# Kernel tuning notes

Measured on AMD Instinct MI355X. Metric: run time of the kernel, lower is better.

Reference implementation:

```python
import jax, jax.numpy as jnp
import numpy as np

NEG_INF = -1e9

def setup_inputs() -> dict:
    key = jax.random.key(0)
    k1, k2, k3, k4, k5 = jax.random.split(key, 5)
    B, Lq, Lk, D = 8, 2048, 2048, 256
    query = jax.random.normal(k1, (B, Lq, D), dtype=jnp.float32)
    key_t = jax.random.normal(k2, (B, Lk, D), dtype=jnp.float32)
    value = jax.random.normal(k3, (B, Lk, D), dtype=jnp.float32)
    mask = jax.random.randint(k4, (B, Lq, Lk), 0, 2, dtype=jnp.int32)
    # nn.Linear(d_k, 1, bias=False) weight, flattened to [d_k]
    w_align = jax.random.normal(k5, (D,), dtype=jnp.float32) / jnp.sqrt(jnp.float32(D))
    return {"query": query, "key": key_t, "value": value, "mask": mask, "w_align": w_align}

def reference(query, key, value, mask, w_align):
    # Bahdanau additive scores: w . (q_i + k_j). Since the alignment layer is
    # linear, distribute it: score[b,i,j] = (q[b,i] . w) + (k[b,j] . w),
    # avoiding the [B,Lq,Lk,D] broadcast intermediate (same math exactly).
    sq = jnp.einsum('bqd,d->bq', query, w_align)   # [B,Lq]
    sk = jnp.einsum('bkd,d->bk', key, w_align)     # [B,Lk]
    scores = sq[:, :, None] + sk[:, None, :]       # [B,Lq,Lk]
    scores = jnp.where(mask == 0, NEG_INF, scores)
    p_attn = jax.nn.softmax(scores, axis=-1)
    return jnp.matmul(p_attn, value)               # [B,Lq,Dv]
```

## Files before the change

### kernel.cpp

```cpp
#include <hip/hip_runtime.h>
#include <hip/hip_bf16.h>


#define NB 8
#define LQ 2048
#define LK 2048
#define DD 256

typedef __attribute__((ext_vector_type(8))) short short8v;
typedef __attribute__((ext_vector_type(8))) unsigned short ushort8v;
typedef __attribute__((ext_vector_type(4))) float f32x4;

__device__ inline unsigned short f2bf(float x) {
  union { __hip_bfloat16 h; unsigned short u; } cv;
  cv.h = __float2bfloat16(x);
  return cv.u;
}

__device__ inline uint4 pack_mask8(const int4 a, const int4 b) {
  uint4 p;
  p.x = (a.x ? 0x3F80u : 0u) | (a.y ? 0x3F800000u : 0u);
  p.y = (a.z ? 0x3F80u : 0u) | (a.w ? 0x3F800000u : 0u);
  p.z = (b.x ? 0x3F80u : 0u) | (b.y ? 0x3F800000u : 0u);
  p.w = (b.z ? 0x3F80u : 0u) | (b.w ? 0x3F800000u : 0u);
  return p;
}

__global__ __launch_bounds__(256) void bah_precompute(
    const float* __restrict__ key, const float* __restrict__ value,
    const float* __restrict__ w, unsigned short* __restrict__ evB,
    unsigned short* __restrict__ eb)
{
  __shared__ float e_s[32];
  __shared__ unsigned short t_s[32][260];

  const int t = threadIdx.x;
  const int lane = t & 63;
  const int wid = t >> 6;
  const int blk = blockIdx.x;
  const int b = blk & 7;
  const int ks = blk >> 3;
  const int j0 = ks * 32;

  const float4 wv4 = reinterpret_cast<const float4*>(w)[lane];

#pragma unroll
  for (int r8 = 0; r8 < 8; ++r8) {
    const int r = wid * 8 + r8;
    const size_t row = (size_t)b * LK + j0 + r;
    const float4 kv = reinterpret_cast<const float4*>(key + row * DD)[lane];
    float s = kv.x * wv4.x + kv.y * wv4.y + kv.z * wv4.z + kv.w * wv4.w;
#pragma unroll
    for (int off = 32; off; off >>= 1) s += __shfl_xor(s, off);
    const float e = __expf(s);
    if (lane == 0) { e_s[r] = e; eb[row] = f2bf(e); }
  }
  __syncthreads();

#pragma unroll
  for (int g = 0; g < 8; ++g) {
    const int jr = g * 4 + wid;
    const int d0 = lane * 4;
    const size_t row = (size_t)b * LK + j0 + jr;
    const float4 vv = reinterpret_cast<const float4*>(value + row * DD)[lane];
    const float e = e_s[jr];
    ushort4 u;
    u.x = f2bf(e * vv.x);
    u.y = f2bf(e * vv.y);
    u.z = f2bf(e * vv.z);
    u.w = f2bf(e * vv.w);
    *reinterpret_cast<ushort4*>(&t_s[jr][d0]) = u;
  }
  __syncthreads();

  const int lr = lane & 15;
  const int lj = lane >> 4;
#pragma unroll
  for (int n4 = 0; n4 < 4; ++n4) {
    const int n = wid * 4 + n4;
    ushort8v va;
#pragma unroll
    for (int i = 0; i < 8; ++i) va[i] = t_s[lj * 8 + i][n * 16 + lr];
    *reinterpret_cast<ushort8v*>(
        evB + ((size_t)((b * 64 + ks) * 16 + n) * 64 + lane) * 8) = va;
  }
}

__global__ __launch_bounds__(256, 2) void bah_gemm(
    const int* __restrict__ mask, const unsigned short* __restrict__ evB,
    const unsigned short* __restrict__ eb, float* __restrict__ out)
{
  __shared__ unsigned short A_s[4][32 * 64];
  __shared__ float denom_s[32];

  const int t = threadIdx.x;
  const int lane = t & 63;
  const int wq = t >> 6;
  const int lr = lane & 15;
  const int lj = lane >> 4;

  const int blk = blockIdx.x;
  const int b = blk & 7;
  const int i0 = (blk >> 3) * 32;

  const int rw = wq * 8 + (lane & 7);
  const int cw = lane >> 3;
  const int* amask = mask + ((size_t)b * LQ + i0 + rw) * LK + cw * 8;
  const int awr = rw * 64 + ((cw ^ (rw & 7)) * 8);

  const unsigned short* bB[4];
#pragma unroll
  for (int n = 0; n < 4; ++n)
    bB[n] = evB + ((size_t)(b * 1024 + (4 * wq + n)) * 64 + lane) * 8;
  const unsigned short* ebb = eb + b * 2048 + lj * 8;

  const int af00 = lr * 64 + (((0 + lj) ^ (lr & 7)) * 8);
  const int af01 = lr * 64 + (((4 + lj) ^ (lr & 7)) * 8);
  const int af10 = (16 + lr) * 64 + (((0 + lj) ^ ((16 + lr) & 7)) * 8);
  const int af11 = (16 + lr) * 64 + (((4 + lj) ^ ((16 + lr) & 7)) * 8);

  f32x4 acc[2][4] = {};
  f32x4 accd0 = {}, accd1 = {};
  const short8v z8 = {};

  {
    const int4 p0 = *reinterpret_cast<const int4*>(amask + 0);
    const int4 p1 = *reinterpret_cast<const int4*>(amask + 4);
    *reinterpret_cast<uint4*>(&A_s[0][awr]) = pack_mask8(p0, p1);
  }
  int4 aC0 = *reinterpret_cast<const int4*>(amask + 64);
  int4 aC1 = *reinterpret_cast<const int4*>(amask + 68);
  __syncthreads();

#pragma unroll 4
  for (int tt = 0; tt < 32; ++tt) {
    const int bufC = tt & 3;
    const int bufW = (tt + 1) & 3;

    short8v bf0[4], bf1[4];
#pragma unroll
    for (int n = 0; n < 4; ++n) {
      bf0[n] = *reinterpret_cast<const short8v*>(bB[n] + (size_t)(2 * tt + 0) * 8192);
      bf1[n] = *reinterpret_cast<const short8v*>(bB[n] + (size_t)(2 * tt + 1) * 8192);
    }
    short8v ef0 = z8, ef1 = z8;
    if (wq == 0) {
      const short8v e0 = *reinterpret_cast<const short8v*>(ebb + (2 * tt + 0) * 32);
      const short8v e1 = *reinterpret_cast<const short8v*>(ebb + (2 * tt + 1) * 32);
      ef0 = (lr == 0) ? e0 : z8;
      ef1 = (lr == 0) ? e1 : z8;
    }
    const int k2 = ((tt + 2) & 31) * 64;
    const int4 aN0 = *reinterpret_cast<const int4*>(amask + k2);
    const int4 aN1 = *reinterpret_cast<const int4*>(amask + k2 + 4);
    __builtin_amdgcn_sched_barrier(0);

    *reinterpret_cast<uint4*>(&A_s[bufW][awr]) = pack_mask8(aC0, aC1);
    asm volatile("s_waitcnt lgkmcnt(0)" ::: "memory");
    __builtin_amdgcn_sched_barrier(0);
    __builtin_amdgcn_s_barrier();
    __builtin_amdgcn_sched_barrier(0);

#pragma unroll
    for (int h = 0; h < 2; ++h) {
      const short8v a0 = *reinterpret_cast<const short8v*>(&A_s[bufC][h ? af01 : af00]);
      const short8v a1 = *reinterpret_cast<const short8v*>(&A_s[bufC][h ? af11 : af10]);
      if (wq == 0) {
        const short8v efh = h ? ef1 : ef0;
        accd0 = __builtin_amdgcn_mfma_f32_16x16x32_bf16(a0, efh, accd0, 0, 0, 0);
        accd1 = __builtin_amdgcn_mfma_f32_16x16x32_bf16(a1, efh, accd1, 0, 0, 0);
      }
#pragma unroll
      for (int n = 0; n < 4; ++n) {
        const short8v bv = h ? bf1[n] : bf0[n];
        acc[0][n] = __builtin_amdgcn_mfma_f32_16x16x32_bf16(a0, bv, acc[0][n], 0, 0, 0);
        acc[1][n] = __builtin_amdgcn_mfma_f32_16x16x32_bf16(a1, bv, acc[1][n], 0, 0, 0);
      }
    }
    aC0 = aN0; aC1 = aN1;
  }

  if (wq == 0 && lr == 0) {
#pragma unroll
    for (int r = 0; r < 4; ++r) {
      denom_s[lj * 4 + r] = accd0[r];
      denom_s[16 + lj * 4 + r] = accd1[r];
    }
  }
  __syncthreads();

#pragma unroll
  for (int m = 0; m < 2; ++m) {
    const int row0 = m * 16 + lj * 4;
    float inv[4];
#pragma unroll
    for (int r = 0; r < 4; ++r) {
      const float dn = denom_s[row0 + r];
      inv[r] = (dn != 0.f) ? 1.f / dn : 0.f;
    }
#pragma unroll
    for (int n = 0; n < 4; ++n) {
      const int col = wq * 64 + n * 16 + lr;
#pragma unroll
      for (int r = 0; r < 4; ++r)
        out[((size_t)b * LQ + (i0 + row0 + r)) * DD + col] = acc[m][n][r] * inv[r];
    }
  }
}

extern "C" void kernel_launch(void* const* d_in, const int* in_sizes, int n_in,
                              void* d_out, int out_size, void* d_ws, size_t ws_size,
                              hipStream_t stream) {
  const float* key   = (const float*)d_in[1];
  const float* value = (const float*)d_in[2];
  const int*   mask  = (const int*)d_in[3];
  const float* w     = (const float*)d_in[4];
  float* out = (float*)d_out;

  unsigned short* evB = (unsigned short*)d_ws;
  unsigned short* eb  = (unsigned short*)((char*)d_ws + (size_t)NB * DD * LK * 2);

  bah_precompute<<<NB * (LK / 32), 256, 0, stream>>>(key, value, w, evB, eb);
  bah_gemm<<<NB * (LQ / 32), 256, 0, stream>>>(mask, evB, eb, out);
}
```

Measured before the change: 55.07 us.

## Split GEMM over key dimension with atomic accumulation and separate normalization pass

The GEMM now uses 64-row tiles with 8 waves (2x4 wave grid) per block and splits the 2048-long key reduction into two halves handled by separate blocks. Partial numerators and denominators are combined with float atomicAdd into the zeroed output and a workspace denominator buffer. A new divide kernel then normalizes each row. This gives more B-operand reuse per block, at the cost of two memsets, atomic traffic on the full output, an extra read-write pass, and non-deterministic summation order.

```diff
diff --git a/kernel.cpp b/kernel.cpp
--- a/kernel.cpp
+++ b/kernel.cpp
@@ -86,57 +86,69 @@
   }
 }
 
-__global__ __launch_bounds__(256, 2) void bah_gemm(
+__global__ __launch_bounds__(512, 4) void bah_gemm(
     const int* __restrict__ mask, const unsigned short* __restrict__ evB,
-    const unsigned short* __restrict__ eb, float* __restrict__ out)
+    const unsigned short* __restrict__ eb, float* __restrict__ out,
+    float* __restrict__ denom)
 {
-  __shared__ unsigned short A_s[4][32 * 64];
-  __shared__ float denom_s[32];
+  __shared__ unsigned short A_s[3][64 * 64];
 
   const int t = threadIdx.x;
   const int lane = t & 63;
-  const int wq = t >> 6;
+  const int wid = t >> 6;
+  const int wm = wid >> 2;
+  const int wn = wid & 3;
   const int lr = lane & 15;
   const int lj = lane >> 4;
 
   const int blk = blockIdx.x;
   const int b = blk & 7;
-  const int i0 = (blk >> 3) * 32;
-
-  const int rw = wq * 8 + (lane & 7);
-  const int cw = lane >> 3;
-  const int* amask = mask + ((size_t)b * LQ + i0 + rw) * LK + cw * 8;
-  const int awr = rw * 64 + ((cw ^ (rw & 7)) * 8);
+  const int r = blk >> 3;
+  const int i0 = (r & 31) * 64;
+  const int s = r >> 5;
+  const int kb = s * 1024;
+
+  const int sr = t >> 3;
+  const int c8 = t & 7;
+  const int* aptr = mask + ((size_t)b * LQ + i0 + sr) * LK + kb + c8 * 8;
+  const int awr = sr * 64 + ((c8 ^ (sr & 7)) * 8);
 
   const unsigned short* bB[4];
 #pragma unroll
   for (int n = 0; n < 4; ++n)
-    bB[n] = evB + ((size_t)(b * 1024 + (4 * wq + n)) * 64 + lane) * 8;
-  const unsigned short* ebb = eb + b * 2048 + lj * 8;
-
-  const int af00 = lr * 64 + (((0 + lj) ^ (lr & 7)) * 8);
-  const int af01 = lr * 64 + (((4 + lj) ^ (lr & 7)) * 8);
-  const int af10 = (16 + lr) * 64 + (((0 + lj) ^ ((16 + lr) & 7)) * 8);
-  const int af11 = (16 + lr) * 64 + (((4 + lj) ^ ((16 + lr) & 7)) * 8);
+    bB[n] = evB + ((size_t)(b * 64 + kb / 32) * 16 + wn * 4 + n) * 512 + lane * 8;
+  const unsigned short* ebb = eb + b * LK + kb + lj * 8;
+
+  int afo[2][2];
+#pragma unroll
+  for (int m = 0; m < 2; ++m) {
+    const int row = wm * 32 + m * 16 + lr;
+#pragma unroll
+    for (int h = 0; h < 2; ++h)
+      afo[m][h] = row * 64 + (((4 * h + lj) ^ (row & 7)) * 8);
+  }
 
   f32x4 acc[2][4] = {};
-  f32x4 accd0 = {}, accd1 = {};
+  f32x4 accd[2] = {};
   const short8v z8 = {};
 
   {
-    const int4 p0 = *reinterpret_cast<const int4*>(amask + 0);
-    const int4 p1 = *reinterpret_cast<const int4*>(amask + 4);
+    const int4 p0 = *reinterpret_cast<const int4*>(aptr);
+    const int4 p1 = *reinterpret_cast<const int4*>(aptr + 4);
     *reinterpret_cast<uint4*>(&A_s[0][awr]) = pack_mask8(p0, p1);
   }
-  int4 aC0 = *reinterpret_cast<const int4*>(amask + 64);
-  int4 aC1 = *reinterpret_cast<const int4*>(amask + 68);
+  int4 aC0 = *reinterpret_cast<const int4*>(aptr + 64);
+  int4 aC1 = *reinterpret_cast<const int4*>(aptr + 68);
   __syncthreads();
 
-#pragma unroll 4
-  for (int tt = 0; tt < 32; ++tt) {
-    const int bufC = tt & 3;
-    const int bufW = (tt + 1) & 3;
-
+#pragma unroll 3
+  for (int tt = 0; tt < 16; ++tt) {
+    const int bufC = tt % 3;
+    const int bufW = (tt + 1) % 3;
+
+    const int k2 = ((tt + 2) & 15) * 64;
+    const int4 aN0 = *reinterpret_cast<const int4*>(aptr + k2);
+    const int4 aN1 = *reinterpret_cast<const int4*>(aptr + k2 + 4);
     short8v bf0[4], bf1[4];
 #pragma unroll
     for (int n = 0; n < 4; ++n) {
@@ -144,15 +156,10 @@
       bf1[n] = *reinterpret_cast<const short8v*>(bB[n] + (size_t)(2 * tt + 1) * 8192);
     }
     short8v ef0 = z8, ef1 = z8;
-    if (wq == 0) {
-      const short8v e0 = *reinterpret_cast<const short8v*>(ebb + (2 * tt + 0) * 32);
-      const short8v e1 = *reinterpret_cast<const short8v*>(ebb + (2 * tt + 1) * 32);
-      ef0 = (lr == 0) ? e0 : z8;
-      ef1 = (lr == 0) ? e1 : z8;
-    }
-    const int k2 = ((tt + 2) & 31) * 64;
-    const int4 aN0 = *reinterpret_cast<const int4*>(amask + k2);
-    const int4 aN1 = *reinterpret_cast<const int4*>(amask + k2 + 4);
+    if (wn == 0 && lr == 0) {
+      ef0 = *reinterpret_cast<const short8v*>(ebb + tt * 64);
+      ef1 = *reinterpret_cast<const short8v*>(ebb + tt * 64 + 32);
+    }
     __builtin_amdgcn_sched_barrier(0);
 
     *reinterpret_cast<uint4*>(&A_s[bufW][awr]) = pack_mask8(aC0, aC1);
@@ -163,12 +170,12 @@
 
 #pragma unroll
     for (int h = 0; h < 2; ++h) {
-      const short8v a0 = *reinterpret_cast<const short8v*>(&A_s[bufC][h ? af01 : af00]);
-      const short8v a1 = *reinterpret_cast<const short8v*>(&A_s[bufC][h ? af11 : af10]);
-      if (wq == 0) {
+      const short8v a0 = *reinterpret_cast<const short8v*>(&A_s[bufC][afo[0][h]]);
+      const short8v a1 = *reinterpret_cast<const short8v*>(&A_s[bufC][afo[1][h]]);
+      if (wn == 0) {
         const short8v efh = h ? ef1 : ef0;
-        accd0 = __builtin_amdgcn_mfma_f32_16x16x32_bf16(a0, efh, accd0, 0, 0, 0);
-        accd1 = __builtin_amdgcn_mfma_f32_16x16x32_bf16(a1, efh, accd1, 0, 0, 0);
+        accd[0] = __builtin_amdgcn_mfma_f32_16x16x32_bf16(a0, efh, accd[0], 0, 0, 0);
+        accd[1] = __builtin_amdgcn_mfma_f32_16x16x32_bf16(a1, efh, accd[1], 0, 0, 0);
       }
 #pragma unroll
       for (int n = 0; n < 4; ++n) {
@@ -180,32 +187,40 @@
     aC0 = aN0; aC1 = aN1;
   }
 
-  if (wq == 0 && lr == 0) {
-#pragma unroll
-    for (int r = 0; r < 4; ++r) {
-      denom_s[lj * 4 + r] = accd0[r];
-      denom_s[16 + lj * 4 + r] = accd1[r];
-    }
-  }
-  __syncthreads();
-
+  if (wn == 0 && lr == 0) {
+#pragma unroll
+    for (int m = 0; m < 2; ++m)
+#pragma unroll
+      for (int rr = 0; rr < 4; ++rr)
+        atomicAdd(denom + b * LQ + i0 + wm * 32 + m * 16 + lj * 4 + rr,
+                  accd[m][rr]);
+  }
 #pragma unroll
   for (int m = 0; m < 2; ++m) {
-    const int row0 = m * 16 + lj * 4;
-    float inv[4];
-#pragma unroll
-    for (int r = 0; r < 4; ++r) {
-      const float dn = denom_s[row0 + r];
-      inv[r] = (dn != 0.f) ? 1.f / dn : 0.f;
-    }
+    const int row0 = wm * 32 + m * 16 + lj * 4;
 #pragma unroll
     for (int n = 0; n < 4; ++n) {
-      const int col = wq * 64 + n * 16 + lr;
-#pragma unroll
-      for (int r = 0; r < 4; ++r)
-        out[((size_t)b * LQ + (i0 + row0 + r)) * DD + col] = acc[m][n][r] * inv[r];
-    }
-  }
+      const int col = wn * 64 + n * 16 + lr;
+#pragma unroll
+      for (int rr = 0; rr < 4; ++rr)
+        atomicAdd(out + ((size_t)b * LQ + i0 + row0 + rr) * DD + col,
+                  acc[m][n][rr]);
+    }
+  }
+}
+
+__global__ __launch_bounds__(256) void bah_divide(
+    float* __restrict__ out, const float* __restrict__ denom)
+{
+  const int t = threadIdx.x;
+  const int row = blockIdx.x * 4 + (t >> 6);
+  const int d4 = (t & 63) * 4;
+  const float dn = denom[row];
+  const float inv = (dn != 0.f) ? 1.f / dn : 0.f;
+  float4* p = reinterpret_cast<float4*>(out + (size_t)row * DD + d4);
+  float4 v = *p;
+  v.x *= inv; v.y *= inv; v.z *= inv; v.w *= inv;
+  *p = v;
 }
 
 extern "C" void kernel_launch(void* const* d_in, const int* in_sizes, int n_in,
@@ -219,7 +234,11 @@
 
   unsigned short* evB = (unsigned short*)d_ws;
   unsigned short* eb  = (unsigned short*)((char*)d_ws + (size_t)NB * DD * LK * 2);
-
+  float* denom = (float*)((char*)d_ws + (size_t)NB * DD * LK * 2 + NB * LK * 2);
+
+  hipMemsetAsync(out, 0, (size_t)NB * LQ * DD * sizeof(float), stream);
+  hipMemsetAsync(denom, 0, (size_t)NB * LQ * sizeof(float), stream);
   bah_precompute<<<NB * (LK / 32), 256, 0, stream>>>(key, value, w, evB, eb);
-  bah_gemm<<<NB * (LQ / 32), 256, 0, stream>>>(mask, evB, eb, out);
-}
+  bah_gemm<<<NB * (LQ / 64) * 2, 512, 0, stream>>>(mask, evB, eb, out, denom);
+  bah_divide<<<NB * LQ / 4, 256, 0, stream>>>(out, denom);
+}
```

After: 84.08 us. 1.53x slower.

## Bit-pack mask in prep kernel and retile GEMM to 64x128 with LDS mask

Applied to the files above, without the earlier changes.

The prep kernel gains extra blocks that compress the int32 mask into 1-bit-per-element words using wave ballots, written to workspace. The GEMM kernel then loads a 64-row packed mask tile into LDS once, expands bits into bf16 A fragments on the fly, and uses a 2x2 wave layout over 64 rows by 128 output columns, with the D dimension split across blocks. This removes the per-iteration LDS write and barrier pipeline for the mask. The cost is that the full int32 mask is still read once in prep, plus an extra write and read of the packed form, and each GEMM block now reads the B operand for only half of D.

```diff
diff --git a/kernel.cpp b/kernel.cpp
--- a/kernel.cpp
+++ b/kernel.cpp
@@ -17,19 +17,11 @@
   return cv.u;
 }
 
-__device__ inline uint4 pack_mask8(const int4 a, const int4 b) {
-  uint4 p;
-  p.x = (a.x ? 0x3F80u : 0u) | (a.y ? 0x3F800000u : 0u);
-  p.y = (a.z ? 0x3F80u : 0u) | (a.w ? 0x3F800000u : 0u);
-  p.z = (b.x ? 0x3F80u : 0u) | (b.y ? 0x3F800000u : 0u);
-  p.w = (b.z ? 0x3F80u : 0u) | (b.w ? 0x3F800000u : 0u);
-  return p;
-}
-
-__global__ __launch_bounds__(256) void bah_precompute(
+__global__ __launch_bounds__(256) void bah_prep(
     const float* __restrict__ key, const float* __restrict__ value,
-    const float* __restrict__ w, unsigned short* __restrict__ evB,
-    unsigned short* __restrict__ eb)
+    const float* __restrict__ w, const int* __restrict__ mask,
+    unsigned short* __restrict__ evB, unsigned short* __restrict__ eb,
+    unsigned int* __restrict__ pmask)
 {
   __shared__ float e_s[32];
   __shared__ unsigned short t_s[32][260];
@@ -38,160 +30,163 @@
   const int lane = t & 63;
   const int wid = t >> 6;
   const int blk = blockIdx.x;
-  const int b = blk & 7;
-  const int ks = blk >> 3;
-  const int j0 = ks * 32;
-
-  const float4 wv4 = reinterpret_cast<const float4*>(w)[lane];
-
-#pragma unroll
-  for (int r8 = 0; r8 < 8; ++r8) {
-    const int r = wid * 8 + r8;
-    const size_t row = (size_t)b * LK + j0 + r;
-    const float4 kv = reinterpret_cast<const float4*>(key + row * DD)[lane];
-    float s = kv.x * wv4.x + kv.y * wv4.y + kv.z * wv4.z + kv.w * wv4.w;
-#pragma unroll
-    for (int off = 32; off; off >>= 1) s += __shfl_xor(s, off);
-    const float e = __expf(s);
-    if (lane == 0) { e_s[r] = e; eb[row] = f2bf(e); }
-  }
-  __syncthreads();
-
-#pragma unroll
-  for (int g = 0; g < 8; ++g) {
-    const int jr = g * 4 + wid;
-    const int d0 = lane * 4;
-    const size_t row = (size_t)b * LK + j0 + jr;
-    const float4 vv = reinterpret_cast<const float4*>(value + row * DD)[lane];
-    const float e = e_s[jr];
-    ushort4 u;
-    u.x = f2bf(e * vv.x);
-    u.y = f2bf(e * vv.y);
-    u.z = f2bf(e * vv.z);
-    u.w = f2bf(e * vv.w);
-    *reinterpret_cast<ushort4*>(&t_s[jr][d0]) = u;
-  }
-  __syncthreads();
-
+
+  if (blk < 512) {
+    const int b = blk & 7;
+    const int ks = blk >> 3;
+    const int j0 = ks * 32;
+
+    const float4 wv4 = reinterpret_cast<const float4*>(w)[lane];
+
+#pragma unroll
+    for (int r8 = 0; r8 < 8; ++r8) {
+      const int r = wid * 8 + r8;
+      const size_t row = (size_t)b * LK + j0 + r;
+      const float4 kv = reinterpret_cast<const float4*>(key + row * DD)[lane];
+      float s = kv.x * wv4.x + kv.y * wv4.y + kv.z * wv4.z + kv.w * wv4.w;
+#pragma unroll
+      for (int off = 32; off; off >>= 1) s += __shfl_xor(s, off);
+      const float e = __expf(s);
+      if (lane == 0) { e_s[r] = e; eb[row] = f2bf(e); }
+    }
+    __syncthreads();
+
+#pragma unroll
+    for (int g = 0; g < 8; ++g) {
+      const int jr = g * 4 + wid;
+      const size_t row = (size_t)b * LK + j0 + jr;
+      const float4 vv = reinterpret_cast<const float4*>(value + row * DD)[lane];
+      const float e = e_s[jr];
+      ushort4 u;
+      u.x = f2bf(e * vv.x);
+      u.y = f2bf(e * vv.y);
+      u.z = f2bf(e * vv.z);
+      u.w = f2bf(e * vv.w);
+      *reinterpret_cast<ushort4*>(&t_s[jr][lane * 4]) = u;
+    }
+    __syncthreads();
+
+    const int lr = lane & 15;
+    const int lj = lane >> 4;
+#pragma unroll
+    for (int n4 = 0; n4 < 4; ++n4) {
+      const int n = wid * 4 + n4;
+      ushort8v va;
+#pragma unroll
+      for (int i = 0; i < 8; ++i) va[i] = t_s[lj * 8 + i][n * 16 + lr];
+      *reinterpret_cast<ushort8v*>(
+          evB + ((size_t)((b * 64 + ks) * 16 + n) * 64 + lane) * 8) = va;
+    }
+  } else {
+    const int gw = (blk - 512) * 4 + wid;
+#pragma unroll 1
+    for (int r4 = 0; r4 < 4; ++r4) {
+      const int rr = gw * 4 + r4;
+      const int* mrow = mask + (size_t)rr * LK;
+      unsigned int myw = 0;
+#pragma unroll
+      for (int c = 0; c < 32; ++c) {
+        const unsigned long long bal = __ballot(mrow[c * 64 + lane] != 0);
+        const unsigned int sel = (lane & 1) ? (unsigned int)(bal >> 32)
+                                            : (unsigned int)bal;
+        myw = ((lane >> 1) == c) ? sel : myw;
+      }
+      pmask[(size_t)rr * 64 + lane] = myw;
+    }
+  }
+}
+
+__global__ __launch_bounds__(256, 2) void bah_gemm(
+    const unsigned int* __restrict__ pmask, const unsigned short* __restrict__ evB,
+    const unsigned short* __restrict__ eb, float* __restrict__ out)
+{
+  __shared__ unsigned int pb_s[64 * 66];
+  __shared__ float denom_s[64];
+
+  const int t = threadIdx.x;
+  const int lane = t & 63;
+  const int wm = (t >> 7) & 1;
+  const int wn = (t >> 6) & 1;
   const int lr = lane & 15;
   const int lj = lane >> 4;
-#pragma unroll
-  for (int n4 = 0; n4 < 4; ++n4) {
-    const int n = wid * 4 + n4;
-    ushort8v va;
-#pragma unroll
-    for (int i = 0; i < 8; ++i) va[i] = t_s[lj * 8 + i][n * 16 + lr];
-    *reinterpret_cast<ushort8v*>(
-        evB + ((size_t)((b * 64 + ks) * 16 + n) * 64 + lane) * 8) = va;
-  }
-}
-
-__global__ __launch_bounds__(256, 2) void bah_gemm(
-    const int* __restrict__ mask, const unsigned short* __restrict__ evB,
-    const unsigned short* __restrict__ eb, float* __restrict__ out)
-{
-  __shared__ unsigned short A_s[4][32 * 64];
-  __shared__ float denom_s[32];
-
-  const int t = threadIdx.x;
-  const int lane = t & 63;
-  const int wq = t >> 6;
-  const int lr = lane & 15;
-  const int lj = lane >> 4;
 
   const int blk = blockIdx.x;
   const int b = blk & 7;
-  const int i0 = (blk >> 3) * 32;
-
-  const int rw = wq * 8 + (lane & 7);
-  const int cw = lane >> 3;
-  const int* amask = mask + ((size_t)b * LQ + i0 + rw) * LK + cw * 8;
-  const int awr = rw * 64 + ((cw ^ (rw & 7)) * 8);
+  const int i0 = ((blk >> 3) & 31) * 64;
+  const int dh = blk >> 8;
+
+  {
+    const unsigned int* src =
+        pmask + ((size_t)(b * LQ + i0 + (t >> 2))) * 64 + (t & 3) * 16;
+    unsigned int* dst = &pb_s[(t >> 2) * 66 + (t & 3) * 16];
+#pragma unroll
+    for (int q = 0; q < 4; ++q)
+      *reinterpret_cast<uint4*>(dst + q * 4) =
+          *reinterpret_cast<const uint4*>(src + q * 4);
+  }
 
   const unsigned short* bB[4];
 #pragma unroll
-  for (int n = 0; n < 4; ++n)
-    bB[n] = evB + ((size_t)(b * 1024 + (4 * wq + n)) * 64 + lane) * 8;
-  const unsigned short* ebb = eb + b * 2048 + lj * 8;
-
-  const int af00 = lr * 64 + (((0 + lj) ^ (lr & 7)) * 8);
-  const int af01 = lr * 64 + (((4 + lj) ^ (lr & 7)) * 8);
-  const int af10 = (16 + lr) * 64 + (((0 + lj) ^ ((16 + lr) & 7)) * 8);
-  const int af11 = (16 + lr) * 64 + (((4 + lj) ^ ((16 + lr) & 7)) * 8);
+  for (int nn = 0; nn < 4; ++nn)
+    bB[nn] = evB + ((size_t)(b * 64) * 16 + dh * 8 + wn * 4 + nn) * 512 + lane * 8;
+  const unsigned short* ebb = eb + b * LK + lj * 8;
 
   f32x4 acc[2][4] = {};
-  f32x4 accd0 = {}, accd1 = {};
+  f32x4 accd[2] = {};
   const short8v z8 = {};
 
-  {
-    const int4 p0 = *reinterpret_cast<const int4*>(amask + 0);
-    const int4 p1 = *reinterpret_cast<const int4*>(amask + 4);
-    *reinterpret_cast<uint4*>(&A_s[0][awr]) = pack_mask8(p0, p1);
-  }
-  int4 aC0 = *reinterpret_cast<const int4*>(amask + 64);
-  int4 aC1 = *reinterpret_cast<const int4*>(amask + 68);
   __syncthreads();
 
-#pragma unroll 4
+#pragma unroll 2
   for (int tt = 0; tt < 32; ++tt) {
-    const int bufC = tt & 3;
-    const int bufW = (tt + 1) & 3;
-
-    short8v bf0[4], bf1[4];
-#pragma unroll
-    for (int n = 0; n < 4; ++n) {
-      bf0[n] = *reinterpret_cast<const short8v*>(bB[n] + (size_t)(2 * tt + 0) * 8192);
-      bf1[n] = *reinterpret_cast<const short8v*>(bB[n] + (size_t)(2 * tt + 1) * 8192);
-    }
-    short8v ef0 = z8, ef1 = z8;
-    if (wq == 0) {
-      const short8v e0 = *reinterpret_cast<const short8v*>(ebb + (2 * tt + 0) * 32);
-      const short8v e1 = *reinterpret_cast<const short8v*>(ebb + (2 * tt + 1) * 32);
-      ef0 = (lr == 0) ? e0 : z8;
-      ef1 = (lr == 0) ? e1 : z8;
-    }
-    const int k2 = ((tt + 2) & 31) * 64;
-    const int4 aN0 = *reinterpret_cast<const int4*>(amask + k2);
-    const int4 aN1 = *reinterpret_cast<const int4*>(amask + k2 + 4);
-    __builtin_amdgcn_sched_barrier(0);
-
-    *reinterpret_cast<uint4*>(&A_s[bufW][awr]) = pack_mask8(aC0, aC1);
-    asm volatile("s_waitcnt lgkmcnt(0)" ::: "memory");
-    __builtin_amdgcn_sched_barrier(0);
-    __builtin_amdgcn_s_barrier();
-    __builtin_amdgcn_sched_barrier(0);
-
 #pragma unroll
     for (int h = 0; h < 2; ++h) {
-      const short8v a0 = *reinterpret_cast<const short8v*>(&A_s[bufC][h ? af01 : af00]);
-      const short8v a1 = *reinterpret_cast<const short8v*>(&A_s[bufC][h ? af11 : af10]);
-      if (wq == 0) {
-        const short8v efh = h ? ef1 : ef0;
-        accd0 = __builtin_amdgcn_mfma_f32_16x16x32_bf16(a0, efh, accd0, 0, 0, 0);
-        accd1 = __builtin_amdgcn_mfma_f32_16x16x32_bf16(a1, efh, accd1, 0, 0, 0);
+      short8v af[2];
+#pragma unroll
+      for (int m = 0; m < 2; ++m) {
+        const int row = wm * 32 + m * 16 + lr;
+        const unsigned int word = pb_s[row * 66 + 2 * tt + h];
+        const unsigned int byte = (word >> (8 * lj)) & 0xFFu;
+        union { uint4 u; short8v s; } ex;
+        ex.u.x = ((byte & 1u)   ? 0x3F80u : 0u) | ((byte & 2u)   ? 0x3F800000u : 0u);
+        ex.u.y = ((byte & 4u)   ? 0x3F80u : 0u) | ((byte & 8u)   ? 0x3F800000u : 0u);
+        ex.u.z = ((byte & 16u)  ? 0x3F80u : 0u) | ((byte & 32u)  ? 0x3F800000u : 0u);
+        ex.u.w = ((byte & 64u)  ? 0x3F80u : 0u) | ((byte & 128u) ? 0x3F800000u : 0u);
+        af[m] = ex.s;
       }
-#pragma unroll
-      for (int n = 0; n < 4; ++n) {
-        const short8v bv = h ? bf1[n] : bf0[n];
-        acc[0][n] = __builtin_amdgcn_mfma_f32_16x16x32_bf16(a0, bv, acc[0][n], 0, 0, 0);
-        acc[1][n] = __builtin_amdgcn_mfma_f32_16x16x32_bf16(a1, bv, acc[1][n], 0, 0, 0);
+      short8v bf[4];
+#pragma unroll
+      for (int nn = 0; nn < 4; ++nn)
+        bf[nn] = *reinterpret_cast<const short8v*>(
+            bB[nn] + (size_t)(2 * tt + h) * 8192);
+      if (wn == 0) {
+        short8v ef = z8;
+        if (lr == 0)
+          ef = *reinterpret_cast<const short8v*>(ebb + tt * 64 + h * 32);
+        accd[0] = __builtin_amdgcn_mfma_f32_16x16x32_bf16(af[0], ef, accd[0], 0, 0, 0);
+        accd[1] = __builtin_amdgcn_mfma_f32_16x16x32_bf16(af[1], ef, accd[1], 0, 0, 0);
       }
-    }
-    aC0 = aN0; aC1 = aN1;
-  }
-
-  if (wq == 0 && lr == 0) {
-#pragma unroll
-    for (int r = 0; r < 4; ++r) {
-      denom_s[lj * 4 + r] = accd0[r];
-      denom_s[16 + lj * 4 + r] = accd1[r];
-    }
+#pragma unroll
+      for (int m = 0; m < 2; ++m)
+#pragma unroll
+        for (int nn = 0; nn < 4; ++nn)
+          acc[m][nn] = __builtin_amdgcn_mfma_f32_16x16x32_bf16(
+              af[m], bf[nn], acc[m][nn], 0, 0, 0);
+    }
+  }
+
+  if (wn == 0 && lr == 0) {
+#pragma unroll
+    for (int m = 0; m < 2; ++m)
+#pragma unroll
+      for (int r = 0; r < 4; ++r)
+        denom_s[wm * 32 + m * 16 + lj * 4 + r] = accd[m][r];
   }
   __syncthreads();
 
 #pragma unroll
   for (int m = 0; m < 2; ++m) {
-    const int row0 = m * 16 + lj * 4;
+    const int row0 = wm * 32 + m * 16 + lj * 4;
     float inv[4];
 #pragma unroll
     for (int r = 0; r < 4; ++r) {
@@ -199,11 +194,11 @@
       inv[r] = (dn != 0.f) ? 1.f / dn : 0.f;
     }
 #pragma unroll
-    for (int n = 0; n < 4; ++n) {
-      const int col = wq * 64 + n * 16 + lr;
+    for (int nn = 0; nn < 4; ++nn) {
+      const int col = dh * 128 + wn * 64 + nn * 16 + lr;
 #pragma unroll
       for (int r = 0; r < 4; ++r)
-        out[((size_t)b * LQ + (i0 + row0 + r)) * DD + col] = acc[m][n][r] * inv[r];
+        out[((size_t)b * LQ + (i0 + row0 + r)) * DD + col] = acc[m][nn][r] * inv[r];
     }
   }
 }
@@ -219,7 +214,9 @@
 
   unsigned short* evB = (unsigned short*)d_ws;
   unsigned short* eb  = (unsigned short*)((char*)d_ws + (size_t)NB * DD * LK * 2);
-
-  bah_precompute<<<NB * (LK / 32), 256, 0, stream>>>(key, value, w, evB, eb);
-  bah_gemm<<<NB * (LQ / 32), 256, 0, stream>>>(mask, evB, eb, out);
-}
+  unsigned int* pmask = (unsigned int*)((char*)d_ws + (size_t)NB * DD * LK * 2
+                                        + (size_t)NB * LK * 2);
+
+  bah_prep<<<1536, 256, 0, stream>>>(key, value, w, mask, evB, eb, pmask);
+  bah_gemm<<<512, 256, 0, stream>>>(pmask, evB, eb, out);
+}
```

After: 68.90 us. +25.1%, slower.
